# Kernel tuning notes

Hardware: AMD Instinct MI355X
Metric: run time of the kernel (lower is better)

The kernel has to match this reference:

```python
import jax, jax.numpy as jnp
import numpy as np

GMIN, GMAX = 0.1, 1.0
DIMS = [3, 256, 256, 256, 1]

def setup_inputs() -> dict:
    key = jax.random.key(0)
    ks = jax.random.split(key, 12)
    inp = {"pos": jax.random.normal(ks[0], (1048576, 3), dtype=jnp.float32)}
    for i in range(4):
        fan_in = DIMS[i]
        bound = 1.0 / np.sqrt(fan_in)
        inp[f"W{i}"] = jax.random.uniform(ks[1 + 2 * i], (fan_in, DIMS[i + 1]), jnp.float32, -bound, bound)
        inp[f"b{i}"] = jax.random.uniform(ks[2 + 2 * i], (DIMS[i + 1],), jnp.float32, -bound, bound)
    for i in range(3):
        inp[f"sigma{i}"] = jax.random.uniform(ks[9 + i], (256,), jnp.float32, GMIN, GMAX)
    return inp

def _gauss(x, sigma):
    # Gaussian activation: exp(-x^2 / (2*sigma^2)), sigma learnable per-feature
    return jnp.exp(-jnp.square(x) / (2.0 * jnp.square(sigma)))

def _softplus8(x):
    # torch Softplus(beta=1, threshold=8): linear beyond threshold
    return jnp.where(x > 8.0, x, jnp.log1p(jnp.exp(jnp.minimum(x, 8.0))))

def reference(pos, W0, b0, W1, b1, W2, b2, W3, b3, sigma0, sigma1, sigma2):
    h = _gauss(pos @ W0 + b0, sigma0)      # [N,256]
    h = _gauss(h @ W1 + b1, sigma1)        # [N,256]
    h = _gauss(h @ W2 + b2, sigma2)        # [N,256]
    return _softplus8(h @ W3 + b3)         # [N,1]
```

## Files before the change

### kernel.cpp

```cpp
#include <hip/hip_runtime.h>
#include <hip/hip_bf16.h>

typedef __attribute__((ext_vector_type(8))) short short8;
typedef __attribute__((ext_vector_type(4))) float f32x4;

#define LOG2E 1.4426950408889634f
#define LN2   0.6931471805599453f

__device__ __forceinline__ unsigned short f2bf(float f) {
    union { float f; unsigned u; } v; v.f = f;
    unsigned u = v.u;
    u += 0x7fffu + ((u >> 16) & 1u);
    return (unsigned short)(u >> 16);
}
__device__ __forceinline__ float bf2f(unsigned short h) {
    union { unsigned u; float f; } v; v.u = ((unsigned)h) << 16;
    return v.f;
}
__device__ __forceinline__ unsigned pk_bf16(float a, float b) {
    __hip_bfloat162 t = __float22bfloat162_rn(float2{a, b});
    union { __hip_bfloat162 b; unsigned u; } v; v.b = t;
    return v.u;
}

__global__ void pack_kernel(const float* __restrict__ W0, const float* __restrict__ W1,
                            const float* __restrict__ W2,
                            const float* __restrict__ s0, const float* __restrict__ s1,
                            const float* __restrict__ s2,
                            unsigned short* __restrict__ wp, float* __restrict__ negc) {
    int tid = blockIdx.x * 256 + threadIdx.x;
    if (tid < 8192) {
        int j = tid & 7, lane = (tid >> 3) & 63, t = tid >> 9;
        int k = ((lane >> 4) * 8) + j;
        int n = ((t >> 1) * 32) + 2 * (lane & 15) + (t & 1);
        unsigned short v = 0;
        if (k < 9) {
            int d = k / 3, m = k - d * 3;
            float w = W0[d * 256 + n];
            unsigned short wh = f2bf(w);
            v = (m == 1) ? f2bf(w - bf2f(wh)) : wh;
        }
        wp[tid] = v;
    } else if (tid < 139264) {
        int e = tid - 8192;
        const float* W = W1;
        if (e >= 65536) { W = W2; e -= 65536; }
        int j = e & 7, lane = (e >> 3) & 63, ks = (e >> 9) & 7, t = e >> 12;
        int k = ks * 32 + ((lane >> 4) * 8) + j;
        int n = ((t >> 1) * 32) + 2 * (lane & 15) + (t & 1);
        wp[tid] = f2bf(W[k * 256 + n]);
    }
    if (tid < 768) {
        const float* s = (tid < 256) ? s0 : (tid < 512 ? s1 : s2);
        float sv = s[tid & 255];
        negc[tid] = -LOG2E / (2.0f * sv * sv);
    }
}

constexpr int ROWS = 128;
constexpr int HSTR = 264;

template <int NKS, int SSTR>
__device__ __forceinline__ void layer(const unsigned short* __restrict__ src,
                                      const unsigned short* __restrict__ wpk,
                                      const float* __restrict__ bias,
                                      const float* __restrict__ ncp,
                                      unsigned short* __restrict__ hdst,
                                      int half, int cq, int i16, int q, bool presync) {
    float2 bp[2], np[2];
#pragma unroll
    for (int p = 0; p < 2; ++p) {
        int ce = cq * 64 + p * 32 + 2 * i16;
        bp[p] = *(const float2*)(bias + ce);
        np[p] = *(const float2*)(ncp + ce);
    }
    f32x4 acc[4][4];
#pragma unroll
    for (int rg = 0; rg < 4; ++rg)
#pragma unroll
        for (int nt = 0; nt < 4; ++nt) {
            float b = (nt & 1) ? bp[nt >> 1].y : bp[nt >> 1].x;
            acc[rg][nt] = f32x4{b, b, b, b};
        }
    const int lane = q * 16 + i16;
    const short8* wp8 = (const short8*)wpk;
    const unsigned short* abase = src + (half * 64 + i16) * SSTR + q * 8;
#pragma unroll
    for (int ks = 0; ks < NKS; ++ks) {
        short8 wf[4];
#pragma unroll
        for (int nt = 0; nt < 4; ++nt)
            wf[nt] = wp8[((cq * 4 + nt) * NKS + ks) * 64 + lane];
#pragma unroll
        for (int rg = 0; rg < 4; ++rg) {
            short8 a = *(const short8*)(abase + rg * 16 * SSTR + ks * 32);
#pragma unroll
            for (int nt = 0; nt < 4; ++nt)
                acc[rg][nt] = __builtin_amdgcn_mfma_f32_16x16x32_bf16(a, wf[nt], acc[rg][nt], 0, 0, 0);
        }
    }
    if (presync) __syncthreads();
#pragma unroll
    for (int rg = 0; rg < 4; ++rg) {
        int row = half * 64 + rg * 16 + q * 4;
#pragma unroll
        for (int p = 0; p < 2; ++p) {
            int col = cq * 64 + p * 32 + 2 * i16;
            float ncx = np[p].x, ncy = np[p].y;
#pragma unroll
            for (int rr = 0; rr < 4; ++rr) {
                float x0 = acc[rg][2 * p][rr];
                float x1 = acc[rg][2 * p + 1][rr];
                float g0 = __builtin_amdgcn_exp2f(x0 * x0 * ncx);
                float g1 = __builtin_amdgcn_exp2f(x1 * x1 * ncy);
                *(unsigned*)&hdst[(row + rr) * HSTR + col] = pk_bf16(g0, g1);
            }
        }
    }
    __syncthreads();
}

__global__ __launch_bounds__(512, 4) void mlp_kernel(
    const float* __restrict__ pos,
    const float* __restrict__ b0, const float* __restrict__ b1,
    const float* __restrict__ b2,
    const float* __restrict__ W3, const float* __restrict__ b3,
    const unsigned short* __restrict__ Wp,
    const float* __restrict__ negc,
    float* __restrict__ out)
{
    __shared__ unsigned short h[ROWS * HSTR];
    __shared__ unsigned short A0[ROWS * 32];

    const int tid  = threadIdx.x;
    const int lane = tid & 63;
    const int wave = tid >> 6;
    const int half = wave >> 2, cq = wave & 3;
    const int i16  = lane & 15, q = lane >> 4;
    const long row0 = (long)blockIdx.x * ROWS;

    if (tid < ROWS) {
        const float* pp = pos + (row0 + tid) * 3;
        float p0 = pp[0], p1 = pp[1], p2 = pp[2];
        short h0 = (short)f2bf(p0); short l0 = (short)f2bf(p0 - bf2f((unsigned short)h0));
        short h1 = (short)f2bf(p1); short l1 = (short)f2bf(p1 - bf2f((unsigned short)h1));
        short h2 = (short)f2bf(p2); short l2 = (short)f2bf(p2 - bf2f((unsigned short)h2));
        short8 s0v = short8{h0, h0, l0, h1, h1, l1, h2, h2};
        short8 s1v = short8{l2, 0, 0, 0, 0, 0, 0, 0};
        short8 zv  = short8{0, 0, 0, 0, 0, 0, 0, 0};
        unsigned short* arow = A0 + tid * 32;
        *(short8*)(arow + 0)  = s0v;
        *(short8*)(arow + 8)  = s1v;
        *(short8*)(arow + 16) = zv;
        *(short8*)(arow + 24) = zv;
    }
    __syncthreads();

    layer<1, 32>(A0, Wp, b0, negc, h, half, cq, i16, q, false);
    layer<8, HSTR>(h, Wp + 8192, b1, negc + 256, h, half, cq, i16, q, true);
    layer<8, HSTR>(h, Wp + 73728, b2, negc + 512, h, half, cq, i16, q, true);

    {
        int r = tid >> 2, qq = tid & 3;
        const unsigned short* hrow = h + r * HSTR + qq * 64;
        const float* w3 = W3 + qq * 64;
        float s = 0.0f;
#pragma unroll
        for (int i = 0; i < 64; i += 8) {
            short8 hv = *(const short8*)(hrow + i);
            f32x4 wA = *(const f32x4*)(w3 + i);
            f32x4 wB = *(const f32x4*)(w3 + i + 4);
#pragma unroll
            for (int jj = 0; jj < 4; ++jj) {
                s = fmaf(bf2f((unsigned short)hv[jj]), wA[jj], s);
                s = fmaf(bf2f((unsigned short)hv[4 + jj]), wB[jj], s);
            }
        }
        s += __shfl_xor(s, 1);
        s += __shfl_xor(s, 2);
        if (qq == 0) {
            float x  = s + b3[0];
            float xm = fminf(x, 8.0f);
            float e  = __builtin_amdgcn_exp2f(xm * LOG2E);
            float sp = __builtin_amdgcn_logf(1.0f + e) * LN2;
            out[row0 + r] = (x > 8.0f) ? x : sp;
        }
    }
}

extern "C" void kernel_launch(void* const* d_in, const int* in_sizes, int n_in,
                              void* d_out, int out_size, void* d_ws, size_t ws_size,
                              hipStream_t stream) {
    const float* pos = (const float*)d_in[0];
    const float* W0  = (const float*)d_in[1];
    const float* b0  = (const float*)d_in[2];
    const float* W1  = (const float*)d_in[3];
    const float* b1  = (const float*)d_in[4];
    const float* W2  = (const float*)d_in[5];
    const float* b2  = (const float*)d_in[6];
    const float* W3  = (const float*)d_in[7];
    const float* b3  = (const float*)d_in[8];
    const float* s0  = (const float*)d_in[9];
    const float* s1  = (const float*)d_in[10];
    const float* s2  = (const float*)d_in[11];

    unsigned short* wp = (unsigned short*)d_ws;
    float* negc = (float*)((char*)d_ws + 278528);

    pack_kernel<<<544, 256, 0, stream>>>(W0, W1, W2, s0, s1, s2, wp, negc);

    int nrows = in_sizes[0] / 3;
    int nblk  = nrows / ROWS;
    mlp_kernel<<<nblk, 512, 0, stream>>>(pos, b0, b1, b2, W3, b3, wp, negc,
                                         (float*)d_out);
}
```

Baseline: 466.2 us.

## Shrink block to 64 rows, 4 waves with 32x128 wave tiles

Cuts the block to 64 rows and 256 threads. Each wave now computes a 32-row by 128-column tile with 8 N-tiles instead of 64x64. The weight packing is reordered so each lane owns 4 adjacent output columns, which allows 8-byte LDS stores of the Gaussian outputs. The layer-0 input stride is padded to 40, and the final dot product interleaves column chunks across the four threads of a row, both to ease LDS bank conflicts. The goal is more resident blocks and better latency hiding, at the cost of more weight-fragment loads per MFMA and lower A reuse per wave.

```diff
diff --git a/kernel.cpp b/kernel.cpp
--- a/kernel.cpp
+++ b/kernel.cpp
@@ -3,6 +3,7 @@
 
 typedef __attribute__((ext_vector_type(8))) short short8;
 typedef __attribute__((ext_vector_type(4))) float f32x4;
+typedef __attribute__((ext_vector_type(2))) unsigned int uint2v;
 
 #define LOG2E 1.4426950408889634f
 #define LN2   0.6931471805599453f
@@ -32,7 +33,7 @@
     if (tid < 8192) {
         int j = tid & 7, lane = (tid >> 3) & 63, t = tid >> 9;
         int k = ((lane >> 4) * 8) + j;
-        int n = ((t >> 1) * 32) + 2 * (lane & 15) + (t & 1);
+        int n = ((t >> 3) * 128) + (((t >> 2) & 1) * 64) + 4 * (lane & 15) + (t & 3);
         unsigned short v = 0;
         if (k < 9) {
             int d = k / 3, m = k - d * 3;
@@ -47,7 +48,7 @@
         if (e >= 65536) { W = W2; e -= 65536; }
         int j = e & 7, lane = (e >> 3) & 63, ks = (e >> 9) & 7, t = e >> 12;
         int k = ks * 32 + ((lane >> 4) * 8) + j;
-        int n = ((t >> 1) * 32) + 2 * (lane & 15) + (t & 1);
+        int n = ((t >> 3) * 128) + (((t >> 2) & 1) * 64) + 4 * (lane & 15) + (t & 3);
         wp[tid] = f2bf(W[k * 256 + n]);
     }
     if (tid < 768) {
@@ -57,8 +58,9 @@
     }
 }
 
-constexpr int ROWS = 128;
+constexpr int ROWS = 64;
 constexpr int HSTR = 264;
+constexpr int ASTR = 40;
 
 template <int NKS, int SSTR>
 __device__ __forceinline__ void layer(const unsigned short* __restrict__ src,
@@ -66,61 +68,64 @@
                                       const float* __restrict__ bias,
                                       const float* __restrict__ ncp,
                                       unsigned short* __restrict__ hdst,
-                                      int half, int cq, int i16, int q, bool presync) {
-    float2 bp[2], np[2];
+                                      int rgrp, int chalf, int i16, int q, bool presync) {
+    f32x4 bb[2], np[2];
 #pragma unroll
     for (int p = 0; p < 2; ++p) {
-        int ce = cq * 64 + p * 32 + 2 * i16;
-        bp[p] = *(const float2*)(bias + ce);
-        np[p] = *(const float2*)(ncp + ce);
-    }
-    f32x4 acc[4][4];
-#pragma unroll
-    for (int rg = 0; rg < 4; ++rg)
-#pragma unroll
-        for (int nt = 0; nt < 4; ++nt) {
-            float b = (nt & 1) ? bp[nt >> 1].y : bp[nt >> 1].x;
+        int ce = chalf * 128 + p * 64 + 4 * i16;
+        bb[p] = *(const f32x4*)(bias + ce);
+        np[p] = *(const f32x4*)(ncp + ce);
+    }
+    f32x4 acc[2][8];
+#pragma unroll
+    for (int rg = 0; rg < 2; ++rg)
+#pragma unroll
+        for (int nt = 0; nt < 8; ++nt) {
+            float b = bb[nt >> 2][nt & 3];
             acc[rg][nt] = f32x4{b, b, b, b};
         }
     const int lane = q * 16 + i16;
     const short8* wp8 = (const short8*)wpk;
-    const unsigned short* abase = src + (half * 64 + i16) * SSTR + q * 8;
+    const unsigned short* abase = src + (rgrp * 32 + i16) * SSTR + q * 8;
 #pragma unroll
     for (int ks = 0; ks < NKS; ++ks) {
-        short8 wf[4];
-#pragma unroll
-        for (int nt = 0; nt < 4; ++nt)
-            wf[nt] = wp8[((cq * 4 + nt) * NKS + ks) * 64 + lane];
-#pragma unroll
-        for (int rg = 0; rg < 4; ++rg) {
+        short8 wf[8];
+#pragma unroll
+        for (int s = 0; s < 8; ++s)
+            wf[s] = wp8[((chalf * 8 + s) * NKS + ks) * 64 + lane];
+#pragma unroll
+        for (int rg = 0; rg < 2; ++rg) {
             short8 a = *(const short8*)(abase + rg * 16 * SSTR + ks * 32);
 #pragma unroll
-            for (int nt = 0; nt < 4; ++nt)
+            for (int nt = 0; nt < 8; ++nt)
                 acc[rg][nt] = __builtin_amdgcn_mfma_f32_16x16x32_bf16(a, wf[nt], acc[rg][nt], 0, 0, 0);
         }
     }
     if (presync) __syncthreads();
-#pragma unroll
-    for (int rg = 0; rg < 4; ++rg) {
-        int row = half * 64 + rg * 16 + q * 4;
+
+#pragma unroll
+    for (int rg = 0; rg < 2; ++rg) {
+        int rbase = rgrp * 32 + rg * 16 + q * 4;
 #pragma unroll
         for (int p = 0; p < 2; ++p) {
-            int col = cq * 64 + p * 32 + 2 * i16;
-            float ncx = np[p].x, ncy = np[p].y;
+            int col = chalf * 128 + p * 64 + 4 * i16;
 #pragma unroll
             for (int rr = 0; rr < 4; ++rr) {
-                float x0 = acc[rg][2 * p][rr];
-                float x1 = acc[rg][2 * p + 1][rr];
-                float g0 = __builtin_amdgcn_exp2f(x0 * x0 * ncx);
-                float g1 = __builtin_amdgcn_exp2f(x1 * x1 * ncy);
-                *(unsigned*)&hdst[(row + rr) * HSTR + col] = pk_bf16(g0, g1);
+                float g0 = __builtin_amdgcn_exp2f(acc[rg][4*p+0][rr] * acc[rg][4*p+0][rr] * np[p][0]);
+                float g1 = __builtin_amdgcn_exp2f(acc[rg][4*p+1][rr] * acc[rg][4*p+1][rr] * np[p][1]);
+                float g2 = __builtin_amdgcn_exp2f(acc[rg][4*p+2][rr] * acc[rg][4*p+2][rr] * np[p][2]);
+                float g3 = __builtin_amdgcn_exp2f(acc[rg][4*p+3][rr] * acc[rg][4*p+3][rr] * np[p][3]);
+                uint2v v;
+                v[0] = pk_bf16(g0, g1);
+                v[1] = pk_bf16(g2, g3);
+                *(uint2v*)&hdst[(rbase + rr) * HSTR + col] = v;
             }
         }
     }
     __syncthreads();
 }
 
-__global__ __launch_bounds__(512, 4) void mlp_kernel(
+__global__ __launch_bounds__(256, 4) void mlp_kernel(
     const float* __restrict__ pos,
     const float* __restrict__ b0, const float* __restrict__ b1,
     const float* __restrict__ b2,
@@ -130,12 +135,12 @@
     float* __restrict__ out)
 {
     __shared__ unsigned short h[ROWS * HSTR];
-    __shared__ unsigned short A0[ROWS * 32];
+    __shared__ unsigned short A0[ROWS * ASTR];
 
     const int tid  = threadIdx.x;
     const int lane = tid & 63;
     const int wave = tid >> 6;
-    const int half = wave >> 2, cq = wave & 3;
+    const int rgrp = wave >> 1, chalf = wave & 1;
     const int i16  = lane & 15, q = lane >> 4;
     const long row0 = (long)blockIdx.x * ROWS;
 
@@ -145,31 +150,28 @@
         short h0 = (short)f2bf(p0); short l0 = (short)f2bf(p0 - bf2f((unsigned short)h0));
         short h1 = (short)f2bf(p1); short l1 = (short)f2bf(p1 - bf2f((unsigned short)h1));
         short h2 = (short)f2bf(p2); short l2 = (short)f2bf(p2 - bf2f((unsigned short)h2));
-        short8 s0v = short8{h0, h0, l0, h1, h1, l1, h2, h2};
-        short8 s1v = short8{l2, 0, 0, 0, 0, 0, 0, 0};
-        short8 zv  = short8{0, 0, 0, 0, 0, 0, 0, 0};
-        unsigned short* arow = A0 + tid * 32;
-        *(short8*)(arow + 0)  = s0v;
-        *(short8*)(arow + 8)  = s1v;
-        *(short8*)(arow + 16) = zv;
-        *(short8*)(arow + 24) = zv;
+        unsigned short* arow = A0 + tid * ASTR;
+        *(short8*)(arow + 0)  = short8{h0, h0, l0, h1, h1, l1, h2, h2};
+        *(short8*)(arow + 8)  = short8{l2, 0, 0, 0, 0, 0, 0, 0};
+        *(short8*)(arow + 16) = short8{0, 0, 0, 0, 0, 0, 0, 0};
+        *(short8*)(arow + 24) = short8{0, 0, 0, 0, 0, 0, 0, 0};
     }
     __syncthreads();
 
-    layer<1, 32>(A0, Wp, b0, negc, h, half, cq, i16, q, false);
-    layer<8, HSTR>(h, Wp + 8192, b1, negc + 256, h, half, cq, i16, q, true);
-    layer<8, HSTR>(h, Wp + 73728, b2, negc + 512, h, half, cq, i16, q, true);
+    layer<1, ASTR>(A0, Wp, b0, negc, h, rgrp, chalf, i16, q, false);
+    layer<8, HSTR>(h, Wp + 8192, b1, negc + 256, h, rgrp, chalf, i16, q, true);
+    layer<8, HSTR>(h, Wp + 73728, b2, negc + 512, h, rgrp, chalf, i16, q, true);
 
     {
         int r = tid >> 2, qq = tid & 3;
-        const unsigned short* hrow = h + r * HSTR + qq * 64;
-        const float* w3 = W3 + qq * 64;
+        const unsigned short* hrow = h + r * HSTR;
         float s = 0.0f;
 #pragma unroll
-        for (int i = 0; i < 64; i += 8) {
-            short8 hv = *(const short8*)(hrow + i);
-            f32x4 wA = *(const f32x4*)(w3 + i);
-            f32x4 wB = *(const f32x4*)(w3 + i + 4);
+        for (int i = 0; i < 8; ++i) {
+            int c = (qq + 4 * i) * 8;
+            short8 hv = *(const short8*)(hrow + c);
+            f32x4 wA = *(const f32x4*)(W3 + c);
+            f32x4 wB = *(const f32x4*)(W3 + c + 4);
 #pragma unroll
             for (int jj = 0; jj < 4; ++jj) {
                 s = fmaf(bf2f((unsigned short)hv[jj]), wA[jj], s);
@@ -211,6 +213,6 @@
 
     int nrows = in_sizes[0] / 3;
     int nblk  = nrows / ROWS;
-    mlp_kernel<<<nblk, 512, 0, stream>>>(pos, b0, b1, b2, W3, b3, wp, negc,
+    mlp_kernel<<<nblk, 256, 0, stream>>>(pos, b0, b1, b2, W3, b3, wp, negc,
                                          (float*)d_out);
 }
```

Measured after the change: 664.6 us. 42.6% more time.
